# Optimization experiments

Hardware: AMD Instinct MI355X
Metric: run time of the kernel (lower is better)

Reference implementation:

```python
import jax, jax.numpy as jnp
import numpy as np

R, D, H, NLAYERS = 128, 64, 64, 3
B, N = 64, 1024
INIT_W = 0.1


def setup_inputs() -> dict:
    key = jax.random.key(0)
    ks = jax.random.split(key, 10)
    x = jax.random.normal(ks[0], (B, D, N), dtype=jnp.float32)
    L = jax.random.randint(ks[1], (B, 1, N), 0, 2, dtype=jnp.int32)
    wq0 = INIT_W * jax.random.normal(ks[2], (R, D), dtype=jnp.float32)
    wqr = INIT_W * jax.random.normal(ks[3], (NLAYERS - 1, R, R), dtype=jnp.float32)
    wk0 = INIT_W * jax.random.normal(ks[4], (R, D), dtype=jnp.float32)
    wkr = INIT_W * jax.random.normal(ks[5], (NLAYERS - 1, R, R), dtype=jnp.float32)
    wv0 = INIT_W * jax.random.normal(ks[6], (R, D), dtype=jnp.float32)
    wvr = INIT_W * jax.random.normal(ks[7], (NLAYERS - 1, R, R), dtype=jnp.float32)
    wor = INIT_W * jax.random.normal(ks[8], (NLAYERS - 1, R, R), dtype=jnp.float32)
    wo_last = INIT_W * jax.random.normal(ks[9], (H, R), dtype=jnp.float32)
    return {"x": x, "L": L, "wq0": wq0, "wqr": wqr, "wk0": wk0, "wkr": wkr,
            "wv0": wv0, "wvr": wvr, "wor": wor, "wo_last": wo_last}


def reference(x, L, wq0, wqr, wk0, wkr, wv0, wvr, wor, wo_last):
    # x: [B, d, N]; L: [B, 1, N] neighbor mask (first row used)
    Lrow = L[:, 0, :].astype(jnp.float32)                      # [B, N]
    num_neighbors = jnp.sum((Lrow >= 1).astype(jnp.float32), axis=1)[:, None, None] + 1.0  # [B,1,1]
    scale = jnp.sqrt(num_neighbors)
    mask = Lrow[:, None, :]                                    # [B, 1, N], broadcast over r

    inp = x
    for layer in range(NLAYERS):
        Wq = wq0 if layer == 0 else wqr[layer - 1]
        Wk = wk0 if layer == 0 else wkr[layer - 1]
        Wv = wv0 if layer == 0 else wvr[layer - 1]
        # sigmoid-gated projections: [B, r, N]
        Q = jax.nn.sigmoid(jnp.einsum('rd,bdn->brn', Wq, inp))
        K = jax.nn.sigmoid(jnp.einsum('rd,bdn->brn', Wk, inp))
        V = jax.nn.sigmoid(jnp.einsum('rd,bdn->brn', Wv, inp))
        # degree-scaled softmax attention over agents: scores [B, N, N]
        A = jax.nn.softmax(jnp.einsum('brn,brm->bnm', Q, K) / scale, axis=-1)
        # o[b,r,n] = sum_m A[b,n,m] * V[b,r,m]  -> [B, r, N]
        o = jnp.einsum('bnm,brm->brn', A, V)
        Wo = wor[layer] if layer < NLAYERS - 1 else wo_last
        inp = jax.nn.silu(jnp.einsum('or,brn->bon', Wo, o))
        if layer != NLAYERS - 1:  # remask_bias=True
            inp = mask * inp
    return inp  # [B, h, N]
```

## Files before the change

### kernel.cpp

```cpp
#include <hip/hip_runtime.h>


typedef __bf16 bf16;
typedef bf16 bf16x2 __attribute__((ext_vector_type(2)));
typedef bf16 bf16x4 __attribute__((ext_vector_type(4)));
typedef bf16 bf16x8 __attribute__((ext_vector_type(8)));
typedef float f32x2 __attribute__((ext_vector_type(2)));
typedef float f32x4 __attribute__((ext_vector_type(4)));
typedef float f32x16 __attribute__((ext_vector_type(16)));

#define MFMA32(a, b, c) __builtin_amdgcn_mfma_f32_32x32x16_bf16(a, b, c, 0, 0, 0)
#define ZERO16 {0,0,0,0,0,0,0,0,0,0,0,0,0,0,0,0}
#define LOG2E 1.44269504f

__device__ __forceinline__ float fast_sigmoid(float x) {
  return __builtin_amdgcn_rcpf(1.0f + exp2f(-LOG2E * x));
}

__global__ __launch_bounds__(256) void prep_kernel(
    const int* __restrict__ L,
    const float* __restrict__ wq0, const float* __restrict__ wqr,
    const float* __restrict__ wk0, const float* __restrict__ wkr,
    const float* __restrict__ wv0, const float* __restrict__ wvr,
    const float* __restrict__ wor, const float* __restrict__ wo_last,
    float* __restrict__ scale_inv, float* __restrict__ biasv,
    bf16* __restrict__ wbf) {
  __shared__ int red[256];
  const int blk = blockIdx.x;
  const int tid = threadIdx.x;
  if (blk < 64) {
    int cnt = 0;
    for (int n = tid; n < 1024; n += 256) cnt += (L[blk * 1024 + n] >= 1) ? 1 : 0;
    red[tid] = cnt;
    __syncthreads();
    for (int s = 128; s > 0; s >>= 1) {
      if (tid < s) red[tid] += red[tid + s];
      __syncthreads();
    }
    if (tid == 0) {
      float iv = rsqrtf((float)red[0] + 1.0f);
      scale_inv[blk] = iv;
      biasv[blk] = fmaxf(0.0f, 128.0f * iv * LOG2E - 80.0f);
    }
  } else {
    for (int i = (blk - 64) * 256 + tid; i < 163840; i += 64 * 256) {
      float v;
      if      (i <   8192) v = wq0[i];
      else if (i <  40960) v = wqr[i - 8192];
      else if (i <  49152) v = wk0[i - 40960];
      else if (i <  81920) v = wkr[i - 49152];
      else if (i <  90112) v = wv0[i - 81920];
      else if (i < 122880) v = wvr[i - 90112];
      else if (i < 155648) v = wor[i - 122880];
      else                 v = wo_last[i - 155648];
      wbf[i] = (bf16)v;
    }
  }
}

__global__ __launch_bounds__(256) void xpose_kernel(const float* __restrict__ x,
                                                    bf16* __restrict__ xT) {
  __shared__ float tile[64][65];
  const int blk = blockIdx.x;
  const int b = blk >> 4;
  const int n0 = (blk & 15) * 64;
  const int tid = threadIdx.x;
  {
    const int nl = tid & 63, dbase = (tid >> 6) * 16;
#pragma unroll
    for (int i = 0; i < 16; i++) {
      int d = dbase + i;
      tile[d][nl] = x[(size_t)(b * 64 + d) * 1024 + n0 + nl];
    }
  }
  __syncthreads();
  {
    const int dl = (tid & 31) * 2, nb = (tid >> 5) * 8;
#pragma unroll
    for (int i = 0; i < 8; i++) {
      int n = nb + i;
      bf16x2 pr = {(bf16)tile[dl][n], (bf16)tile[dl + 1][n]};
      *(bf16x2*)(xT + (size_t)(b * 1024 + n0 + n) * 64 + dl) = pr;
    }
  }
}

template <int DIN>
__global__ __launch_bounds__(256) void kv_kernel(
    const bf16* __restrict__ inpT, const bf16* __restrict__ Wk,
    const bf16* __restrict__ Wv, bf16* __restrict__ Kt,
    bf16* __restrict__ Vn) {
  constexpr int SIN = DIN + 8;
  constexpr int KS = DIN / 16;
  constexpr int CPR = DIN / 8;
  __shared__ __attribute__((aligned(16))) bf16 inp_lds[64 * SIN];
  const int tid = threadIdx.x;
  const int lane = tid & 63, wv = tid >> 6;
  const int la = lane & 31, hi = lane >> 5;
  const int b = blockIdx.x >> 4;
  const int t0 = (blockIdx.x & 15) * 64;

  for (int i = tid; i < 64 * CPR; i += 256) {
    int row = i / CPR, c = i % CPR;
    *(bf16x8*)&inp_lds[row * SIN + c * 8] =
        *(const bf16x8*)(inpT + (size_t)(b * 1024 + t0 + row) * DIN + c * 8);
  }
  __syncthreads();

  const int sub = wv & 1;
  if (wv < 2) {
#pragma unroll
    for (int rt2 = 0; rt2 < 2; rt2++) {
      const int rt = 2 * sub + rt2;
      bf16x8 wf[KS];
#pragma unroll
      for (int ks = 0; ks < KS; ks++)
        wf[ks] = *(const bf16x8*)(Wk + (size_t)(la + 32 * rt) * DIN + hi * 8 + ks * 16);
#pragma unroll
      for (int tt = 0; tt < 2; tt++) {
        f32x16 acc = ZERO16;
#pragma unroll
        for (int ks = 0; ks < KS; ks++) {
          bf16x8 bfr = *(const bf16x8*)&inp_lds[(la + 32 * tt) * SIN + hi * 8 + ks * 16];
          acc = MFMA32(wf[ks], bfr, acc);
        }
#pragma unroll
        for (int g = 0; g < 4; g++) {
          bf16x4 pk;
#pragma unroll
          for (int i = 0; i < 4; i++) pk[i] = (bf16)fast_sigmoid(acc[4 * g + i]);
          *(bf16x4*)(Kt + (size_t)(b * 1024 + t0 + 32 * tt + la) * 128 +
                     32 * rt + 8 * g + 4 * hi) = pk;
        }
      }
    }
  } else {
#pragma unroll
    for (int rc2 = 0; rc2 < 2; rc2++) {
      const int rc = 2 * sub + rc2;
      bf16x8 wf[KS];
#pragma unroll
      for (int ks = 0; ks < KS; ks++)
        wf[ks] = *(const bf16x8*)(Wv + (size_t)(la + 32 * rc) * DIN + hi * 8 + ks * 16);
#pragma unroll
      for (int tt = 0; tt < 2; tt++) {
        f32x16 acc = ZERO16;
#pragma unroll
        for (int ks = 0; ks < KS; ks++) {
          bf16x8 afr = *(const bf16x8*)&inp_lds[(la + 32 * tt) * SIN + hi * 8 + ks * 16];
          acc = MFMA32(afr, wf[ks], acc);
        }
#pragma unroll
        for (int g = 0; g < 4; g++) {
          bf16x4 pk;
#pragma unroll
          for (int i = 0; i < 4; i++) pk[i] = (bf16)fast_sigmoid(acc[4 * g + i]);
          *(bf16x4*)(Vn + (size_t)(b * 128 + la + 32 * rc) * 1024 +
                     t0 + 32 * tt + 8 * g + 4 * hi) = pk;
        }
      }
    }
  }
}

template <int DIN>
__global__ __launch_bounds__(256, 2) void flash_kernel(
    const bf16* __restrict__ inpT, const bf16* __restrict__ Wq,
    const bf16* __restrict__ Kt, const bf16* __restrict__ Vn,
    const float* __restrict__ scale_inv, const float* __restrict__ biasv,
    const int* __restrict__ L, const bf16* __restrict__ Wo,
    void* __restrict__ outp, int last) {
  __shared__ __attribute__((aligned(16))) char smem[70656];
  bf16* K_lds = (bf16*)smem;
  bf16* V_lds = (bf16*)(smem + 17408);
  bf16* P_lds = (bf16*)(smem + 35840);

  const int tid = threadIdx.x;
  const int lane = tid & 63, wv = tid >> 6;
  const int la = lane & 31, hi = lane >> 5;
  const int b = blockIdx.x >> 3;
  const int q0 = (blockIdx.x & 7) * 128;

  const float inv2 = scale_inv[b] * LOG2E;
  const float bb = biasv[b];

  {
    constexpr int SIN = DIN + 8;
    constexpr int KSD = DIN / 16;
    constexpr int CPR = DIN / 8;
    bf16* inp_s = (bf16*)smem;
    for (int i = tid; i < 128 * CPR; i += 256) {
      int row = i / CPR, c = i % CPR;
      *(bf16x8*)&inp_s[row * SIN + c * 8] =
          *(const bf16x8*)(inpT + (size_t)(b * 1024 + q0 + row) * DIN + c * 8);
    }
    __syncthreads();
    bf16* Q_lds = (bf16*)(smem + 35840);
    bf16x8 wf[KSD];
#pragma unroll
    for (int ks = 0; ks < KSD; ks++)
      wf[ks] = *(const bf16x8*)(Wq + (size_t)(la + 32 * wv) * DIN + hi * 8 + ks * 16);
#pragma unroll
    for (int nt = 0; nt < 4; nt++) {
      f32x16 acc = ZERO16;
#pragma unroll
      for (int ks = 0; ks < KSD; ks++) {
        bf16x8 bfr = *(const bf16x8*)&inp_s[(la + 32 * nt) * SIN + hi * 8 + ks * 16];
        acc = MFMA32(wf[ks], bfr, acc);
      }
#pragma unroll
      for (int g = 0; g < 4; g++) {
        bf16x4 pk;
#pragma unroll
        for (int i = 0; i < 4; i++)
          pk[i] = (bf16)(fast_sigmoid(acc[4 * g + i]) * inv2);
        *(bf16x4*)&Q_lds[(size_t)(32 * nt + la) * 136 + 32 * wv + 8 * g + 4 * hi] = pk;
      }
    }
    __syncthreads();
  }

  const int ms = wv & 1, nw = wv >> 1;
  bf16x8 qB[2][8];
#pragma unroll
  for (int nt = 0; nt < 2; nt++)
#pragma unroll
    for (int ks = 0; ks < 8; ks++)
      qB[nt][ks] = *(const bf16x8*)((bf16*)(smem + 35840) +
                                    (size_t)(64 * nw + 32 * nt + la) * 136 +
                                    hi * 8 + ks * 16);

  const int krow = tid >> 4, kc = (tid & 15) * 8;
  const int vrow = tid >> 3, vc = (tid & 7) * 8;
  const bf16* kbase = Kt + (size_t)b * 1024 * 128;
  const bf16* vbase = Vn + (size_t)b * 128 * 1024;
  bf16x8 kr[4], vr[4];
#pragma unroll
  for (int p = 0; p < 4; p++) {
    kr[p] = *(const bf16x8*)(kbase + (size_t)(krow + 16 * p) * 128 + kc);
    vr[p] = *(const bf16x8*)(vbase + (size_t)(vrow + 32 * p) * 1024 + vc);
  }

  const int nh = wv & 1, rh = wv >> 1;
  f32x16 acc_o[2][2] = {{ZERO16, ZERO16}, {ZERO16, ZERO16}};
  float rs[2] = {0.f, 0.f};

  for (int it = 0; it < 16; it++) {
    __syncthreads();
#pragma unroll
    for (int p = 0; p < 4; p++)
      *(bf16x8*)&K_lds[(krow + 16 * p) * 136 + kc] = kr[p];
#pragma unroll
    for (int p = 0; p < 4; p++)
      *(bf16x8*)&V_lds[(vrow + 32 * p) * 72 + vc] = vr[p];
    __syncthreads();

    if (it < 15) {
      const int m1 = (it + 1) * 64;
#pragma unroll
      for (int p = 0; p < 4; p++) {
        kr[p] = *(const bf16x8*)(kbase + (size_t)(m1 + krow + 16 * p) * 128 + kc);
        vr[p] = *(const bf16x8*)(vbase + (size_t)(vrow + 32 * p) * 1024 + m1 + vc);
      }
    }

    bf16x8 kf[8];
#pragma unroll
    for (int ks = 0; ks < 8; ks++)
      kf[ks] = *(const bf16x8*)&K_lds[(32 * ms + la) * 136 + hi * 8 + ks * 16];
#pragma unroll
    for (int nt = 0; nt < 2; nt++) {
      f32x16 sa = ZERO16;
#pragma unroll
      for (int ks = 0; ks < 8; ks++) sa = MFMA32(kf[ks], qB[nt][ks], sa);
#pragma unroll
      for (int g = 0; g < 4; g++) {
        bf16x4 pk;
#pragma unroll
        for (int i = 0; i < 4; i++) {
          float p = exp2f(sa[4 * g + i] - bb);
          rs[nt] += p;
          pk[i] = (bf16)p;
        }
        *(bf16x4*)&P_lds[(size_t)(64 * nw + 32 * nt + la) * 72 +
                         32 * ms + 8 * g + 4 * hi] = pk;
      }
    }
    __syncthreads();

    bf16x8 pA[2][4];
#pragma unroll
    for (int nt2 = 0; nt2 < 2; nt2++)
#pragma unroll
      for (int k2 = 0; k2 < 4; k2++)
        pA[nt2][k2] = *(const bf16x8*)&P_lds[(size_t)(64 * nh + 32 * nt2 + la) * 72 +
                                             hi * 8 + k2 * 16];
#pragma unroll
    for (int rt = 0; rt < 2; rt++) {
#pragma unroll
      for (int k2 = 0; k2 < 4; k2++) {
        bf16x8 vB = *(const bf16x8*)&V_lds[(size_t)(64 * rh + 32 * rt + la) * 72 +
                                           hi * 8 + k2 * 16];
        acc_o[0][rt] = MFMA32(pA[0][k2], vB, acc_o[0][rt]);
        acc_o[1][rt] = MFMA32(pA[1][k2], vB, acc_o[1][rt]);
      }
    }
  }

  rs[0] += __shfl_xor(rs[0], 32, 64);
  rs[1] += __shfl_xor(rs[1], 32, 64);
  __syncthreads();
  float* rsp = (float*)smem;
  if (lane < 32) {
    rsp[ms * 128 + 64 * nw + la] = rs[0];
    rsp[ms * 128 + 64 * nw + 32 + la] = rs[1];
  }
  float* Lm = (float*)(smem + 1024);
  if (!last && tid < 128) Lm[tid] = (float)L[b * 1024 + q0 + tid];
  __syncthreads();

  bf16* O_lds = (bf16*)(smem + 35840);
#pragma unroll
  for (int nt2 = 0; nt2 < 2; nt2++) {
#pragma unroll
    for (int g = 0; g < 4; g++) {
      const int nb = 64 * nh + 32 * nt2 + 8 * g + 4 * hi;
      f32x4 ra = *(f32x4*)&rsp[nb];
      f32x4 rc = *(f32x4*)&rsp[128 + nb];
      f32x4 is;
#pragma unroll
      for (int i = 0; i < 4; i++) is[i] = 1.0f / (ra[i] + rc[i]);
#pragma unroll
      for (int rt = 0; rt < 2; rt++) {
#pragma unroll
        for (int i = 0; i < 4; i++) {
          O_lds[(size_t)(nb + i) * 136 + 64 * rh + 32 * rt + la] =
              (bf16)(acc_o[nt2][rt][4 * g + i] * is[i]);
        }
      }
    }
  }
  __syncthreads();

  if (!last) {
    bf16* out_b = (bf16*)outp;
    bf16x8 wB[8];
#pragma unroll
    for (int ks = 0; ks < 8; ks++)
      wB[ks] = *(const bf16x8*)(Wo + (size_t)(la + 32 * wv) * 128 + hi * 8 + ks * 16);
#pragma unroll
    for (int nt = 0; nt < 4; nt++) {
      f32x16 acc = ZERO16;
#pragma unroll
      for (int ks = 0; ks < 8; ks++) {
        bf16x8 oA = *(const bf16x8*)&O_lds[(size_t)(la + 32 * nt) * 136 +
                                           hi * 8 + ks * 16];
        acc = MFMA32(oA, wB[ks], acc);
      }
#pragma unroll
      for (int g = 0; g < 4; g++) {
#pragma unroll
        for (int i = 0; i < 4; i++) {
          int n = 32 * nt + 8 * g + 4 * hi + i;
          float xv = acc[4 * g + i];
          float y = xv * fast_sigmoid(xv) * Lm[n];
          out_b[(size_t)(b * 1024 + q0 + n) * 128 + 32 * wv + la] = (bf16)y;
        }
      }
    }
  } else {
    const int hs = wv & 1, nq = wv >> 1;
    float* outf = (float*)outp;
    bf16x8 wA[8];
#pragma unroll
    for (int ks = 0; ks < 8; ks++)
      wA[ks] = *(const bf16x8*)(Wo + (size_t)(la + 32 * hs) * 128 + hi * 8 + ks * 16);
#pragma unroll
    for (int t = 0; t < 2; t++) {
      const int ns4 = nq + 2 * t;
      f32x16 acc = ZERO16;
#pragma unroll
      for (int ks = 0; ks < 8; ks++) {
        bf16x8 oB = *(const bf16x8*)&O_lds[(size_t)(32 * ns4 + la) * 136 +
                                           hi * 8 + ks * 16];
        acc = MFMA32(wA[ks], oB, acc);
      }
#pragma unroll
      for (int g = 0; g < 4; g++) {
#pragma unroll
        for (int i = 0; i < 4; i++) {
          int h = 32 * hs + 8 * g + 4 * hi + i;
          float xv = acc[4 * g + i];
          outf[(size_t)(b * 64 + h) * 1024 + q0 + 32 * ns4 + la] =
              xv * fast_sigmoid(xv);
        }
      }
    }
  }
}

extern "C" void kernel_launch(void* const* d_in, const int* in_sizes, int n_in,
                              void* d_out, int out_size, void* d_ws, size_t ws_size,
                              hipStream_t stream) {
  const float* x = (const float*)d_in[0];
  const int* L = (const int*)d_in[1];
  const float* wq0 = (const float*)d_in[2];
  const float* wqr = (const float*)d_in[3];
  const float* wk0 = (const float*)d_in[4];
  const float* wkr = (const float*)d_in[5];
  const float* wv0 = (const float*)d_in[6];
  const float* wvr = (const float*)d_in[7];
  const float* wor = (const float*)d_in[8];
  const float* wo_last = (const float*)d_in[9];

  char* ws = (char*)d_ws;
  float* scale_inv = (float*)(ws + 0);
  float* biasv = (float*)(ws + 1024);
  bf16* wbf = (bf16*)(ws + 4096);
  bf16* xT = (bf16*)(ws + 335872);
  bf16* inpT = (bf16*)(ws + 8724480);
  bf16* Kt = (bf16*)(ws + 25501696);
  bf16* Vn = (bf16*)(ws + 42278912);
  if (ws_size < 59056128) return;

  prep_kernel<<<128, 256, 0, stream>>>(L, wq0, wqr, wk0, wkr, wv0, wvr, wor,
                                       wo_last, scale_inv, biasv, wbf);
  xpose_kernel<<<1024, 256, 0, stream>>>(x, xT);

  for (int l = 0; l < 3; l++) {
    const bf16* Wq = (l == 0) ? wbf + 0 : wbf + 8192 + (size_t)(l - 1) * 16384;
    const bf16* Wk = (l == 0) ? wbf + 40960 : wbf + 49152 + (size_t)(l - 1) * 16384;
    const bf16* Wv = (l == 0) ? wbf + 81920 : wbf + 90112 + (size_t)(l - 1) * 16384;
    const bf16* Wo = (l < 2) ? wbf + 122880 + (size_t)l * 16384 : wbf + 155648;
    void* outp = (l < 2) ? (void*)inpT : (void*)d_out;
    if (l == 0) {
      kv_kernel<64><<<1024, 256, 0, stream>>>(xT, Wk, Wv, Kt, Vn);
      flash_kernel<64><<<512, 256, 0, stream>>>(xT, Wq, Kt, Vn, scale_inv,
                                                biasv, L, Wo, outp, 0);
    } else {
      kv_kernel<128><<<1024, 256, 0, stream>>>(inpT, Wk, Wv, Kt, Vn);
      flash_kernel<128><<<512, 256, 0, stream>>>(inpT, Wq, Kt, Vn, scale_inv,
                                                 biasv, L, Wo, outp,
                                                 (l == 2) ? 1 : 0);
    }
  }
}
```

Before: 334.5 us.

## Fuse next-layer K/V projection into flash epilogue and transpose into layer-0 KV

The layer-0 K/V projection is folded into the transpose kernel. Each flash kernel now also computes the next layer's sigmoid K and V from its freshly produced output tile held in LDS, writing into double-buffered K/V workspaces. This removes the separate kv_kernel launches and the re-read of the intermediate activations from global memory. In exchange it needs a larger workspace, with a fallback to the old path when the workspace is too small, and the flash kernel gets a heavier epilogue that raises register pressure and serial work per block. Inside flash_kernel, inpT is overwritten while other blocks may still read it, but each block reads only its own query rows, so this looks safe.

```diff
diff --git a/kernel.cpp b/kernel.cpp
--- a/kernel.cpp
+++ b/kernel.cpp
@@ -5,7 +5,6 @@
 typedef bf16 bf16x2 __attribute__((ext_vector_type(2)));
 typedef bf16 bf16x4 __attribute__((ext_vector_type(4)));
 typedef bf16 bf16x8 __attribute__((ext_vector_type(8)));
-typedef float f32x2 __attribute__((ext_vector_type(2)));
 typedef float f32x4 __attribute__((ext_vector_type(4)));
 typedef float f32x16 __attribute__((ext_vector_type(16)));
 
@@ -58,19 +57,24 @@
   }
 }
 
-__global__ __launch_bounds__(256) void xpose_kernel(const float* __restrict__ x,
-                                                    bf16* __restrict__ xT) {
+__global__ __launch_bounds__(256) void xk0_kernel(
+    const float* __restrict__ x, const bf16* __restrict__ Wk,
+    const bf16* __restrict__ Wv, bf16* __restrict__ xT,
+    bf16* __restrict__ Kt, bf16* __restrict__ Vn) {
   __shared__ float tile[64][65];
-  const int blk = blockIdx.x;
-  const int b = blk >> 4;
-  const int n0 = (blk & 15) * 64;
+  __shared__ __attribute__((aligned(16))) bf16 inp_lds[64 * 72];
   const int tid = threadIdx.x;
+  const int lane = tid & 63, wv = tid >> 6;
+  const int la = lane & 31, hi = lane >> 5;
+  const int b = blockIdx.x >> 4;
+  const int t0 = (blockIdx.x & 15) * 64;
+
   {
     const int nl = tid & 63, dbase = (tid >> 6) * 16;
 #pragma unroll
     for (int i = 0; i < 16; i++) {
       int d = dbase + i;
-      tile[d][nl] = x[(size_t)(b * 64 + d) * 1024 + n0 + nl];
+      tile[d][nl] = x[(size_t)(b * 64 + d) * 1024 + t0 + nl];
     }
   }
   __syncthreads();
@@ -80,7 +84,64 @@
     for (int i = 0; i < 8; i++) {
       int n = nb + i;
       bf16x2 pr = {(bf16)tile[dl][n], (bf16)tile[dl + 1][n]};
-      *(bf16x2*)(xT + (size_t)(b * 1024 + n0 + n) * 64 + dl) = pr;
+      *(bf16x2*)(xT + (size_t)(b * 1024 + t0 + n) * 64 + dl) = pr;
+      *(bf16x2*)&inp_lds[n * 72 + dl] = pr;
+    }
+  }
+  __syncthreads();
+
+  const int sub = wv & 1;
+  if (wv < 2) {
+#pragma unroll
+    for (int rt2 = 0; rt2 < 2; rt2++) {
+      const int rt = 2 * sub + rt2;
+      bf16x8 wf[4];
+#pragma unroll
+      for (int ks = 0; ks < 4; ks++)
+        wf[ks] = *(const bf16x8*)(Wk + (size_t)(la + 32 * rt) * 64 + hi * 8 + ks * 16);
+#pragma unroll
+      for (int tt = 0; tt < 2; tt++) {
+        f32x16 acc = ZERO16;
+#pragma unroll
+        for (int ks = 0; ks < 4; ks++) {
+          bf16x8 bfr = *(const bf16x8*)&inp_lds[(la + 32 * tt) * 72 + hi * 8 + ks * 16];
+          acc = MFMA32(wf[ks], bfr, acc);
+        }
+#pragma unroll
+        for (int g = 0; g < 4; g++) {
+          bf16x4 pk;
+#pragma unroll
+          for (int i = 0; i < 4; i++) pk[i] = (bf16)fast_sigmoid(acc[4 * g + i]);
+          *(bf16x4*)(Kt + (size_t)(b * 1024 + t0 + 32 * tt + la) * 128 +
+                     32 * rt + 8 * g + 4 * hi) = pk;
+        }
+      }
+    }
+  } else {
+#pragma unroll
+    for (int rc2 = 0; rc2 < 2; rc2++) {
+      const int rc = 2 * sub + rc2;
+      bf16x8 wf[4];
+#pragma unroll
+      for (int ks = 0; ks < 4; ks++)
+        wf[ks] = *(const bf16x8*)(Wv + (size_t)(la + 32 * rc) * 64 + hi * 8 + ks * 16);
+#pragma unroll
+      for (int tt = 0; tt < 2; tt++) {
+        f32x16 acc = ZERO16;
+#pragma unroll
+        for (int ks = 0; ks < 4; ks++) {
+          bf16x8 afr = *(const bf16x8*)&inp_lds[(la + 32 * tt) * 72 + hi * 8 + ks * 16];
+          acc = MFMA32(afr, wf[ks], acc);
+        }
+#pragma unroll
+        for (int g = 0; g < 4; g++) {
+          bf16x4 pk;
+#pragma unroll
+          for (int i = 0; i < 4; i++) pk[i] = (bf16)fast_sigmoid(acc[4 * g + i]);
+          *(bf16x4*)(Vn + (size_t)(b * 128 + la + 32 * rc) * 1024 +
+                     t0 + 32 * tt + 8 * g + 4 * hi) = pk;
+        }
+      }
     }
   }
 }
@@ -169,7 +230,9 @@
     const bf16* __restrict__ Kt, const bf16* __restrict__ Vn,
     const float* __restrict__ scale_inv, const float* __restrict__ biasv,
     const int* __restrict__ L, const bf16* __restrict__ Wo,
-    void* __restrict__ outp, int last) {
+    void* __restrict__ outp, int last,
+    const bf16* __restrict__ Wkn, const bf16* __restrict__ Wvn,
+    bf16* __restrict__ Ktn, bf16* __restrict__ Vnn, int kvgen) {
   __shared__ __attribute__((aligned(16))) char smem[70656];
   bf16* K_lds = (bf16*)smem;
   bf16* V_lds = (bf16*)(smem + 17408);
@@ -315,8 +378,6 @@
     rsp[ms * 128 + 64 * nw + la] = rs[0];
     rsp[ms * 128 + 64 * nw + 32 + la] = rs[1];
   }
-  float* Lm = (float*)(smem + 1024);
-  if (!last && tid < 128) Lm[tid] = (float)L[b * 1024 + q0 + tid];
   __syncthreads();
 
   bf16* O_lds = (bf16*)(smem + 35840);
@@ -344,6 +405,8 @@
 
   if (!last) {
     bf16* out_b = (bf16*)outp;
+    bf16* O2 = (bf16*)smem;
+    const int* Lg = L + b * 1024 + q0;
     bf16x8 wB[8];
 #pragma unroll
     for (int ks = 0; ks < 8; ks++)
@@ -363,8 +426,58 @@
         for (int i = 0; i < 4; i++) {
           int n = 32 * nt + 8 * g + 4 * hi + i;
           float xv = acc[4 * g + i];
-          float y = xv * fast_sigmoid(xv) * Lm[n];
+          float y = xv * fast_sigmoid(xv) * (float)Lg[n];
           out_b[(size_t)(b * 1024 + q0 + n) * 128 + 32 * wv + la] = (bf16)y;
+          if (kvgen) O2[(size_t)n * 136 + 32 * wv + la] = (bf16)y;
+        }
+      }
+    }
+    if (kvgen) {
+      __syncthreads();
+      const int sub = wv & 1;
+      const bf16* W2 = (wv < 2) ? Wkn : Wvn;
+#pragma unroll
+      for (int rt2 = 0; rt2 < 2; rt2++) {
+        const int rt = 2 * sub + rt2;
+        bf16x8 wf[8];
+#pragma unroll
+        for (int ks = 0; ks < 8; ks++)
+          wf[ks] = *(const bf16x8*)(W2 + (size_t)(la + 32 * rt) * 128 +
+                                    hi * 8 + ks * 16);
+#pragma unroll
+        for (int tt = 0; tt < 4; tt++) {
+          f32x16 acc = ZERO16;
+          if (wv < 2) {
+#pragma unroll
+            for (int ks = 0; ks < 8; ks++) {
+              bf16x8 bB = *(const bf16x8*)&O2[(size_t)(32 * tt + la) * 136 +
+                                              hi * 8 + ks * 16];
+              acc = MFMA32(wf[ks], bB, acc);
+            }
+#pragma unroll
+            for (int g = 0; g < 4; g++) {
+              bf16x4 pk;
+#pragma unroll
+              for (int i = 0; i < 4; i++) pk[i] = (bf16)fast_sigmoid(acc[4 * g + i]);
+              *(bf16x4*)(Ktn + (size_t)(b * 1024 + q0 + 32 * tt + la) * 128 +
+                         32 * rt + 8 * g + 4 * hi) = pk;
+            }
+          } else {
+#pragma unroll
+            for (int ks = 0; ks < 8; ks++) {
+              bf16x8 aA = *(const bf16x8*)&O2[(size_t)(32 * tt + la) * 136 +
+                                              hi * 8 + ks * 16];
+              acc = MFMA32(aA, wf[ks], acc);
+            }
+#pragma unroll
+            for (int g = 0; g < 4; g++) {
+              bf16x4 pk;
+#pragma unroll
+              for (int i = 0; i < 4; i++) pk[i] = (bf16)fast_sigmoid(acc[4 * g + i]);
+              *(bf16x4*)(Vnn + (size_t)(b * 128 + 32 * rt + la) * 1024 +
+                         q0 + 32 * tt + 8 * g + 4 * hi) = pk;
+            }
+          }
         }
       }
     }
@@ -395,6 +508,33 @@
               xv * fast_sigmoid(xv);
         }
       }
+    }
+  }
+}
+
+__global__ __launch_bounds__(256) void xpose_kernel(const float* __restrict__ x,
+                                                    bf16* __restrict__ xT) {
+  __shared__ float tile[64][65];
+  const int blk = blockIdx.x;
+  const int b = blk >> 4;
+  const int n0 = (blk & 15) * 64;
+  const int tid = threadIdx.x;
+  {
+    const int nl = tid & 63, dbase = (tid >> 6) * 16;
+#pragma unroll
+    for (int i = 0; i < 16; i++) {
+      int d = dbase + i;
+      tile[d][nl] = x[(size_t)(b * 64 + d) * 1024 + n0 + nl];
+    }
+  }
+  __syncthreads();
+  {
+    const int dl = (tid & 31) * 2, nb = (tid >> 5) * 8;
+#pragma unroll
+    for (int i = 0; i < 8; i++) {
+      int n = nb + i;
+      bf16x2 pr = {(bf16)tile[dl][n], (bf16)tile[dl + 1][n]};
+      *(bf16x2*)(xT + (size_t)(b * 1024 + n0 + n) * 64 + dl) = pr;
     }
   }
 }
@@ -419,29 +559,46 @@
   bf16* wbf = (bf16*)(ws + 4096);
   bf16* xT = (bf16*)(ws + 335872);
   bf16* inpT = (bf16*)(ws + 8724480);
-  bf16* Kt = (bf16*)(ws + 25501696);
-  bf16* Vn = (bf16*)(ws + 42278912);
-  if (ws_size < 59056128) return;
+  bf16* KtA = (bf16*)(ws + 25501696);
+  bf16* VnA = (bf16*)(ws + 42278912);
+  bf16* KtB = (bf16*)(ws + 59056128);
+  bf16* VnB = (bf16*)(ws + 75833344);
 
   prep_kernel<<<128, 256, 0, stream>>>(L, wq0, wqr, wk0, wkr, wv0, wvr, wor,
                                        wo_last, scale_inv, biasv, wbf);
-  xpose_kernel<<<1024, 256, 0, stream>>>(x, xT);
-
-  for (int l = 0; l < 3; l++) {
-    const bf16* Wq = (l == 0) ? wbf + 0 : wbf + 8192 + (size_t)(l - 1) * 16384;
-    const bf16* Wk = (l == 0) ? wbf + 40960 : wbf + 49152 + (size_t)(l - 1) * 16384;
-    const bf16* Wv = (l == 0) ? wbf + 81920 : wbf + 90112 + (size_t)(l - 1) * 16384;
-    const bf16* Wo = (l < 2) ? wbf + 122880 + (size_t)l * 16384 : wbf + 155648;
-    void* outp = (l < 2) ? (void*)inpT : (void*)d_out;
-    if (l == 0) {
-      kv_kernel<64><<<1024, 256, 0, stream>>>(xT, Wk, Wv, Kt, Vn);
-      flash_kernel<64><<<512, 256, 0, stream>>>(xT, Wq, Kt, Vn, scale_inv,
-                                                biasv, L, Wo, outp, 0);
-    } else {
-      kv_kernel<128><<<1024, 256, 0, stream>>>(inpT, Wk, Wv, Kt, Vn);
-      flash_kernel<128><<<512, 256, 0, stream>>>(inpT, Wq, Kt, Vn, scale_inv,
-                                                 biasv, L, Wo, outp,
-                                                 (l == 2) ? 1 : 0);
+
+  if (ws_size >= 92610560) {
+    xk0_kernel<<<1024, 256, 0, stream>>>(x, wbf + 40960, wbf + 81920, xT, KtA, VnA);
+    flash_kernel<64><<<512, 256, 0, stream>>>(
+        xT, wbf + 0, KtA, VnA, scale_inv, biasv, L, wbf + 122880, (void*)inpT, 0,
+        wbf + 49152, wbf + 90112, KtB, VnB, 1);
+    flash_kernel<128><<<512, 256, 0, stream>>>(
+        inpT, wbf + 8192, KtB, VnB, scale_inv, biasv, L, wbf + 139264,
+        (void*)inpT, 0, wbf + 65536, wbf + 106496, KtA, VnA, 1);
+    flash_kernel<128><<<512, 256, 0, stream>>>(
+        inpT, wbf + 24576, KtA, VnA, scale_inv, biasv, L, wbf + 155648, d_out, 1,
+        nullptr, nullptr, nullptr, nullptr, 0);
+  } else if (ws_size >= 59056128) {
+    xpose_kernel<<<1024, 256, 0, stream>>>(x, xT);
+    for (int l = 0; l < 3; l++) {
+      const bf16* Wq = (l == 0) ? wbf + 0 : wbf + 8192 + (size_t)(l - 1) * 16384;
+      const bf16* Wk = (l == 0) ? wbf + 40960 : wbf + 49152 + (size_t)(l - 1) * 16384;
+      const bf16* Wv = (l == 0) ? wbf + 81920 : wbf + 90112 + (size_t)(l - 1) * 16384;
+      const bf16* Wo = (l < 2) ? wbf + 122880 + (size_t)l * 16384 : wbf + 155648;
+      void* outp = (l < 2) ? (void*)inpT : (void*)d_out;
+      if (l == 0) {
+        kv_kernel<64><<<1024, 256, 0, stream>>>(xT, Wk, Wv, KtA, VnA);
+        flash_kernel<64><<<512, 256, 0, stream>>>(xT, Wq, KtA, VnA, scale_inv,
+                                                  biasv, L, Wo, outp, 0,
+                                                  nullptr, nullptr, nullptr,
+                                                  nullptr, 0);
+      } else {
+        kv_kernel<128><<<1024, 256, 0, stream>>>(inpT, Wk, Wv, KtA, VnA);
+        flash_kernel<128><<<512, 256, 0, stream>>>(inpT, Wq, KtA, VnA, scale_inv,
+                                                   biasv, L, Wo, outp,
+                                                   (l == 2) ? 1 : 0, nullptr,
+                                                   nullptr, nullptr, nullptr, 0);
+      }
     }
   }
 }
```

New measurement: 324.2 us. 1.03x faster.
